# Performance work log

Hardware: AMD Instinct MI355X
Metric: run time of the kernel (lower is better)

Reference implementation:

```python
import jax, jax.numpy as jnp
import numpy as np

B = 524288
H = 20          # heads
NUM_EX = 13     # embedding rows
EMB = 3         # embedding dim
FEAT_IN, FEAT_OUT = 3, 5
HEAD_IN, HEAD_HID = 8, 10


def setup_inputs() -> dict:
    key = jax.random.key(0)
    ks = jax.random.split(key, 12)
    e = jax.random.randint(ks[0], (B, H), 0, NUM_EX)
    f = jax.random.normal(ks[1], (B, H * FEAT_IN), dtype=jnp.float32)
    # embedding table; row 0 zeroed as in the torch __init__
    emb = jax.random.normal(ks[2], (NUM_EX, EMB), dtype=jnp.float32) * 0.1
    emb = emb.at[0].set(0.0)
    # features Linear(3 -> 5), stored as (in, out) so y = x @ Wf + bf
    Wf = jax.random.normal(ks[3], (FEAT_IN, FEAT_OUT), dtype=jnp.float32) * 0.5
    bf = jax.random.normal(ks[4], (FEAT_OUT,), dtype=jnp.float32) * 0.1
    # 20 parallel head MLPs, batched over the head axis
    W1 = jax.random.normal(ks[5], (H, HEAD_IN, HEAD_HID), dtype=jnp.float32) * 0.3
    b1 = jax.random.normal(ks[6], (H, HEAD_HID), dtype=jnp.float32) * 0.1
    W2 = jax.random.normal(ks[7], (H, HEAD_HID), dtype=jnp.float32) * 0.3
    b2 = jax.random.normal(ks[8], (H,), dtype=jnp.float32) * 0.1
    # output Linear(20 -> 1)
    Wo = jax.random.normal(ks[9], (H, 1), dtype=jnp.float32) * 0.3
    bo = jax.random.normal(ks[10], (1,), dtype=jnp.float32) * 0.1
    return {"e": e, "f": f, "emb": emb, "Wf": Wf, "bf": bf,
            "W1": W1, "b1": b1, "W2": W2, "b2": b2, "Wo": Wo, "bo": bo}


def reference(e, f, emb, Wf, bf, W1, b1, W2, b2, Wo, bo):
    ev = emb[e]                                    # (B, 20, 3) embedding lookup
    fv = f.reshape(-1, H, FEAT_IN) @ Wf + bf       # (B, 20, 5)
    x = jnp.concatenate([ev, fv], axis=2)          # (B, 20, 8)
    # all 20 heads as one batched matmul instead of a Python loop
    h1 = jax.nn.leaky_relu(jnp.einsum('bhi,hio->bho', x, W1) + b1)  # (B, 20, 10)
    h = jax.nn.softplus(jnp.einsum('bho,ho->bh', h1, W2) + b2)      # (B, 20)
    return h @ Wo + bo                             # (B, 1)
```

## Files before the change

kernel.cpp:

```cpp
#include <hip/hip_runtime.h>


#define HH   20
#define NEX  13
#define NT   512

#define WS_T   0
#define WS_M   1560
#define WS_WB  1880
#define WS_END 2040

typedef _Float16 hv2 __attribute__((ext_vector_type(2)));

__device__ __forceinline__ float softplus_fast(float x) {
    return fmaxf(x, 0.0f) + __logf(1.0f + __expf(-fabsf(x)));
}

__device__ __forceinline__ float fdot2f(hv2 a, hv2 b, float c) {
#if __has_builtin(__builtin_amdgcn_fdot2)
    return __builtin_amdgcn_fdot2(a, b, c, false);
#else
    return fmaf((float)a.x, (float)b.x, fmaf((float)a.y, (float)b.y, c));
#endif
}

__device__ __forceinline__ hv2 cvt_pk(float x, float y) {
#if __has_builtin(__builtin_amdgcn_cvt_pkrtz)
    return __builtin_bit_cast(hv2, __builtin_amdgcn_cvt_pkrtz(x, y));
#else
    return hv2{ (_Float16)x, (_Float16)y };
#endif
}

__global__ void airfit_setup(const float* __restrict__ emb,
                             const float* __restrict__ Wf,
                             const float* __restrict__ bf,
                             const float* __restrict__ W1,
                             const float* __restrict__ b1,
                             const float* __restrict__ W2,
                             const float* __restrict__ b2,
                             const float* __restrict__ Wo,
                             float* __restrict__ ws)
{
    int t = blockIdx.x * 256 + threadIdx.x;
    hv2* wsh = reinterpret_cast<hv2*>(ws);

    if (t < HH * NEX * 6) {
        int h = t / (NEX * 6), r = t % (NEX * 6), idx = r / 6, p = r % 6;
        float v[2] = { 0.0f, 0.0f };
        if (p < 5) {
            for (int s = 0; s < 2; ++s) {
                int o = 2 * p + s;
                float a = b1[h * 10 + o];
                for (int i = 0; i < 3; ++i)
                    a += emb[idx * 3 + i] * W1[(h * 8 + i) * 10 + o];
                for (int q = 0; q < 5; ++q)
                    a += bf[q] * W1[(h * 8 + 3 + q) * 10 + o];
                v[s] = a;
            }
        }
        wsh[WS_T + t] = hv2{ (_Float16)v[0], (_Float16)v[1] };
    }
    if (t < HH * 16) {
        int h = t / 16, s = t % 16;
        float v[2] = { 0.0f, 0.0f };
        if (s < 15) {
            int c = s / 5, pp = s % 5;
            for (int sd = 0; sd < 2; ++sd) {
                int o = 2 * pp + sd;
                float a = 0.0f;
                for (int q = 0; q < 5; ++q)
                    a += Wf[c * 5 + q] * W1[(h * 8 + 3 + q) * 10 + o];
                v[sd] = a;
            }
        }
        wsh[WS_M + t] = hv2{ (_Float16)v[0], (_Float16)v[1] };
    }
    if (t < HH * 8) {
        int h = t / 8, s = t % 8;
        float outv = 0.0f;
        if (s < 5)
            outv = __builtin_bit_cast(float,
                       hv2{ (_Float16)W2[h * 10 + 2 * s],
                            (_Float16)W2[h * 10 + 2 * s + 1] });
        else if (s == 5) outv = b2[h];
        else if (s == 6) outv = Wo[h];
        ws[WS_WB + t] = outv;
    }
}

__global__ __launch_bounds__(NT, 6) void airfit_kernel(
    const int*   __restrict__ e,   const float* __restrict__ f,
    const float* __restrict__ ws,  const float* __restrict__ bo,
    float* __restrict__ out, int B)
{
    __shared__ __align__(16) float s_c[WS_END];

    const int tid  = threadIdx.x;
    const int base = blockIdx.x * NT;
    const int nIt  = min(NT, B - base);

    for (int t = tid; t < WS_END; t += NT) s_c[t] = ws[t];
    __syncthreads();

    if (tid >= nIt) return;
    const int item = base + tid;

    const int4* eg = reinterpret_cast<const int4*>(e + (size_t)item * HH);
    int4 e0 = eg[0], e1 = eg[1], e2 = eg[2], e3 = eg[3], e4 = eg[4];
    unsigned ew0 = (unsigned)(e0.x & 15)        | ((unsigned)(e0.y & 15) << 4)
                 | ((unsigned)(e0.z & 15) << 8) | ((unsigned)(e0.w & 15) << 12)
                 | ((unsigned)(e1.x & 15) << 16)| ((unsigned)(e1.y & 15) << 20)
                 | ((unsigned)(e1.z & 15) << 24)| ((unsigned)(e1.w & 15) << 28);
    unsigned ew1 = (unsigned)(e2.x & 15)        | ((unsigned)(e2.y & 15) << 4)
                 | ((unsigned)(e2.z & 15) << 8) | ((unsigned)(e2.w & 15) << 12)
                 | ((unsigned)(e3.x & 15) << 16)| ((unsigned)(e3.y & 15) << 20)
                 | ((unsigned)(e3.z & 15) << 24)| ((unsigned)(e3.w & 15) << 28);
    unsigned ew2 = (unsigned)(e4.x & 15)        | ((unsigned)(e4.y & 15) << 4)
                 | ((unsigned)(e4.z & 15) << 8) | ((unsigned)(e4.w & 15) << 12);

    const float4* fg = reinterpret_cast<const float4*>(f + (size_t)item * 60);
    hv2 fh[30];
#pragma unroll
    for (int k = 0; k < 15; ++k) {
        float4 v = fg[k];
        fh[2 * k]     = cvt_pk(v.x, v.y);
        fh[2 * k + 1] = cvt_pk(v.z, v.w);
    }

    const hv2* Tt = reinterpret_cast<const hv2*>(s_c + WS_T);
    const hv2* Mt = reinterpret_cast<const hv2*>(s_c + WS_M);
    const hv2 lk2 = hv2{ (_Float16)0.01f, (_Float16)0.01f };

    float acc = bo[0];
#pragma unroll
    for (int h = 0; h < HH; ++h) {
        unsigned word = (h < 8) ? ew0 : ((h < 16) ? ew1 : ew2);
        int idx = (int)((word >> (4 * (h & 7))) & 0xfu);

        const hv2* Tr = Tt + (h * NEX + idx) * 6;
        hv2 tp[5] = { Tr[0], Tr[1], Tr[2], Tr[3], Tr[4] };

        const int kb = (3 * h) >> 1;
        _Float16 x0, x1, x2;
        if ((h & 1) == 0) { x0 = fh[kb].x;  x1 = fh[kb].y;   x2 = fh[kb+1].x; }
        else              { x0 = fh[kb].y;  x1 = fh[kb+1].x; x2 = fh[kb+1].y; }
        hv2 g0 = hv2{ x0, x0 }, g1 = hv2{ x1, x1 }, g2 = hv2{ x2, x2 };

        const hv2*   Mh  = Mt + h * 16;
        const float* wb  = s_c + WS_WB + h * 8;
        const hv2*   W2h = reinterpret_cast<const hv2*>(wb);

        float hacc = wb[5];
#pragma unroll
        for (int p = 0; p < 5; ++p) {
            hv2 v = g0 * Mh[p] + tp[p];
            v = g1 * Mh[5 + p] + v;
            v = g2 * Mh[10 + p] + v;
            v = __builtin_elementwise_max(v, v * lk2);
            hacc = fdot2f(v, W2h[p], hacc);
        }
        acc = fmaf(softplus_fast(hacc), wb[6], acc);
    }

    out[item] = acc;
}

extern "C" void kernel_launch(void* const* d_in, const int* in_sizes, int n_in,
                              void* d_out, int out_size, void* d_ws, size_t ws_size,
                              hipStream_t stream) {
    const int*   e   = (const int*)  d_in[0];
    const float* f   = (const float*)d_in[1];
    const float* emb = (const float*)d_in[2];
    const float* Wf  = (const float*)d_in[3];
    const float* bf  = (const float*)d_in[4];
    const float* W1  = (const float*)d_in[5];
    const float* b1  = (const float*)d_in[6];
    const float* W2  = (const float*)d_in[7];
    const float* b2  = (const float*)d_in[8];
    const float* Wo  = (const float*)d_in[9];
    const float* bo  = (const float*)d_in[10];
    float* out = (float*)d_out;
    float* ws  = (float*)d_ws;

    int B = in_sizes[0] / HH;

    int sblocks = (HH * NEX * 6 + 255) / 256;
    airfit_setup<<<sblocks, 256, 0, stream>>>(emb, Wf, bf, W1, b1, W2, b2, Wo, ws);

    int blocks = (B + NT - 1) / NT;
    airfit_kernel<<<blocks, NT, 0, stream>>>(e, f, ws, bo, out, B);
}
```

Before: 246.3 us.

## Stream f in per-group chunks, vectorize LDS weight loads, raise occupancy bound

Restructures the head loop into 5 groups of 4 heads and loads only the 12 floats of f each group needs, just before use, instead of converting all 60 up front into a 30-element register array. This cuts live registers, and the launch bound minimum blocks per CU is raised from 6 to 8 to take advantage. The per-head M and W2/bias reads from shared memory become float4 vector loads. The trade-off is that the global loads of f are spread across the loop rather than issued all at once, which may reduce memory-level parallelism per thread.

After: 258.8 us. 1.05x slower.

```diff
diff --git a/kernel.cpp b/kernel.cpp
--- a/kernel.cpp
+++ b/kernel.cpp
@@ -89,7 +89,7 @@
     }
 }
 
-__global__ __launch_bounds__(NT, 6) void airfit_kernel(
+__global__ __launch_bounds__(NT, 8) void airfit_kernel(
     const int*   __restrict__ e,   const float* __restrict__ f,
     const float* __restrict__ ws,  const float* __restrict__ bo,
     float* __restrict__ out, int B)
@@ -120,47 +120,57 @@
                  | ((unsigned)(e4.z & 15) << 8) | ((unsigned)(e4.w & 15) << 12);
 
     const float4* fg = reinterpret_cast<const float4*>(f + (size_t)item * 60);
-    hv2 fh[30];
+    const hv2*    Tt = reinterpret_cast<const hv2*>(s_c + WS_T);
+    const hv2 lk2 = hv2{ (_Float16)0.01f, (_Float16)0.01f };
+
+    float acc = bo[0];
+
 #pragma unroll
-    for (int k = 0; k < 15; ++k) {
-        float4 v = fg[k];
-        fh[2 * k]     = cvt_pk(v.x, v.y);
-        fh[2 * k + 1] = cvt_pk(v.z, v.w);
-    }
-
-    const hv2* Tt = reinterpret_cast<const hv2*>(s_c + WS_T);
-    const hv2* Mt = reinterpret_cast<const hv2*>(s_c + WS_M);
-    const hv2 lk2 = hv2{ (_Float16)0.01f, (_Float16)0.01f };
-
-    float acc = bo[0];
+    for (int gq = 0; gq < 5; ++gq) {
+        float4 fa = fg[3 * gq], fb = fg[3 * gq + 1], fc4 = fg[3 * gq + 2];
+        hv2 fc[6] = { cvt_pk(fa.x, fa.y), cvt_pk(fa.z, fa.w),
+                      cvt_pk(fb.x, fb.y), cvt_pk(fb.z, fb.w),
+                      cvt_pk(fc4.x, fc4.y), cvt_pk(fc4.z, fc4.w) };
+
+        unsigned ewx = (gq < 2) ? ew0 : ((gq < 4) ? ew1 : ew2);
+        unsigned gw  = (gq & 1) ? (ewx >> 16) : ewx;
+
 #pragma unroll
-    for (int h = 0; h < HH; ++h) {
-        unsigned word = (h < 8) ? ew0 : ((h < 16) ? ew1 : ew2);
-        int idx = (int)((word >> (4 * (h & 7))) & 0xfu);
-
-        const hv2* Tr = Tt + (h * NEX + idx) * 6;
-        hv2 tp[5] = { Tr[0], Tr[1], Tr[2], Tr[3], Tr[4] };
-
-        const int kb = (3 * h) >> 1;
-        _Float16 x0, x1, x2;
-        if ((h & 1) == 0) { x0 = fh[kb].x;  x1 = fh[kb].y;   x2 = fh[kb+1].x; }
-        else              { x0 = fh[kb].y;  x1 = fh[kb+1].x; x2 = fh[kb+1].y; }
-        hv2 g0 = hv2{ x0, x0 }, g1 = hv2{ x1, x1 }, g2 = hv2{ x2, x2 };
-
-        const hv2*   Mh  = Mt + h * 16;
-        const float* wb  = s_c + WS_WB + h * 8;
-        const hv2*   W2h = reinterpret_cast<const hv2*>(wb);
-
-        float hacc = wb[5];
+        for (int t = 0; t < 4; ++t) {
+            const int h = 4 * gq + t;
+            int idx = (int)((gw >> (4 * t)) & 0xfu);
+
+            const hv2* Tr = Tt + (h * NEX + idx) * 6;
+            hv2 tp[5] = { Tr[0], Tr[1], Tr[2], Tr[3], Tr[4] };
+
+            const float4* Mh4 =
+                reinterpret_cast<const float4*>(s_c + WS_M + h * 16);
+            float4 m0 = Mh4[0], m1 = Mh4[1], m2 = Mh4[2], m3 = Mh4[3];
+            float mj[16] = { m0.x, m0.y, m0.z, m0.w,  m1.x, m1.y, m1.z, m1.w,
+                             m2.x, m2.y, m2.z, m2.w,  m3.x, m3.y, m3.z, m3.w };
+
+            const float4* wb4 =
+                reinterpret_cast<const float4*>(s_c + WS_WB + h * 8);
+            float4 w0 = wb4[0], w1 = wb4[1];
+            float wj[5] = { w0.x, w0.y, w0.z, w0.w, w1.x };
+
+            const int kb = (3 * t) >> 1;
+            _Float16 x0, x1, x2;
+            if ((t & 1) == 0) { x0 = fc[kb].x;  x1 = fc[kb].y;   x2 = fc[kb+1].x; }
+            else              { x0 = fc[kb].y;  x1 = fc[kb+1].x; x2 = fc[kb+1].y; }
+            hv2 g0 = hv2{ x0, x0 }, g1 = hv2{ x1, x1 }, g2 = hv2{ x2, x2 };
+
+            float hacc = w1.y;
 #pragma unroll
-        for (int p = 0; p < 5; ++p) {
-            hv2 v = g0 * Mh[p] + tp[p];
-            v = g1 * Mh[5 + p] + v;
-            v = g2 * Mh[10 + p] + v;
-            v = __builtin_elementwise_max(v, v * lk2);
-            hacc = fdot2f(v, W2h[p], hacc);
+            for (int p = 0; p < 5; ++p) {
+                hv2 v = g0 * __builtin_bit_cast(hv2, mj[p])      + tp[p];
+                v = g1 * __builtin_bit_cast(hv2, mj[5 + p])  + v;
+                v = g2 * __builtin_bit_cast(hv2, mj[10 + p]) + v;
+                v = __builtin_elementwise_max(v, v * lk2);
+                hacc = fdot2f(v, __builtin_bit_cast(hv2, wj[p]), hacc);
+            }
+            acc = fmaf(softplus_fast(hacc), w1.z, acc);
         }
-        acc = fmaf(softplus_fast(hacc), wb[6], acc);
     }
 
     out[item] = acc;
```
